# Optimization experiments

Hardware: AMD Instinct MI355X
Metric: run time of the kernel (lower is better)

Reference implementation:

```python
import jax, jax.numpy as jnp
import numpy as np

L = 3000          # nodes per modality
M = 3             # modalities
N = L * M         # total nodes
E = 200000        # edges
D = 512           # hidden_dim
S = D // 4        # shared_dim = 128
EPS = 1e-12       # F.normalize eps


def _lrelu(x):
    return jax.nn.leaky_relu(x, negative_slope=0.01)


def _l2norm(x):
    n = jnp.linalg.norm(x, axis=-1, keepdims=True)
    return x / jnp.maximum(n, EPS)


def setup_inputs() -> dict:
    key = jax.random.key(0)
    ks = jax.random.split(key, 16)
    w = lambda k, shape: (jax.random.normal(k, shape, dtype=jnp.float32) * 0.02)
    inp = {
        "feat0": jax.random.normal(ks[0], (L, D), dtype=jnp.float32),
        "feat1": jax.random.normal(ks[1], (L, D), dtype=jnp.float32),
        "feat2": jax.random.normal(ks[2], (L, D), dtype=jnp.float32),
        "edge_index": jax.random.randint(ks[3], (2, E), 0, N, dtype=jnp.int64),
        # EdgeWeightGen params (torch Linear convention: weight is (out, in))
        "proj_w": w(ks[4], (S, D)),
        "mlp_w1": w(ks[5], (S, 2 * S)),
        "mlp_b1": jnp.zeros((S,), dtype=jnp.float32),
        "mlp_w2": w(ks[6], (1, S)),
        "mlp_b2": jnp.zeros((1,), dtype=jnp.float32),
        # CrossModalGraphLayer params, 2 layers
        "W1_0": w(ks[7], (D, D)),
        "W2_0": w(ks[8], (D, 2 * D)),
        "W1_1": w(ks[9], (D, D)),
        "W2_1": w(ks[10], (D, 2 * D)),
    }
    return inp


def reference(feat0, feat1, feat2, edge_index, proj_w, mlp_w1, mlp_b1,
              mlp_w2, mlp_b2, W1_0, W2_0, W1_1, W2_1):
    feature = jnp.concatenate([feat0, feat1, feat2], axis=0)  # (N, D)
    src, tgt = edge_index[0], edge_index[1]

    # EdgeWeightGen
    shared_src = _l2norm(feature[src] @ proj_w.T)   # (E, S)
    shared_tgt = _l2norm(feature[tgt] @ proj_w.T)   # (E, S)
    emb_cat = jnp.concatenate([shared_src, shared_tgt], axis=-1)  # (E, 2S)
    h = _lrelu(emb_cat @ mlp_w1.T + mlp_b1)
    edge_weight = jax.nn.sigmoid((h @ mlp_w2.T + mlp_b2)[:, 0])   # (E,)

    # build_adj_matrix: dense scatter-add (sparse_coo coalesce sums dups)
    adj = jnp.zeros((N, N), dtype=feature.dtype).at[src, tgt].add(edge_weight)
    row_sum = adj.sum(axis=1)
    d_inv_sqrt = jnp.where(row_sum > 0, row_sum ** -0.5, 0.0)
    # D^{-1/2} A D^{-1/2} as elementwise row/col scaling (same math as diag matmuls)
    gcn = d_inv_sqrt[:, None] * adj * d_inv_sqrt[None, :]

    # graph layers
    x = feature
    for W1, W2 in ((W1_0, W2_0), (W1_1, W2_1)):
        proj = x @ W1.T                 # (N, D)
        nb = gcn @ proj                 # (N, D)
        cat = jnp.concatenate([x + nb, x * nb], axis=-1)  # (N, 2D)
        x = _lrelu(cat @ W2.T)
    return x  # concatenated updated features; chunk(x, 3) recovers per-modal tuple
```

## Files before the change

kernel.cpp:

```cpp
#include <hip/hip_runtime.h>
#include <hip/hip_bf16.h>
#include <math.h>

#define NL 3000
#define NN 9000
#define NE 200000
#define DD 512
#define SS 128
#define MPAD 9088
#define MT   (MPAD/16)

typedef __attribute__((ext_vector_type(8))) short    bf16x8;
typedef __attribute__((ext_vector_type(8))) ushort   u16x8;
typedef __attribute__((ext_vector_type(4))) float    f32x4;

static __device__ __forceinline__ ushort f2bf(float f){
  unsigned u = __float_as_uint(f);
  return (ushort)((u + 0x7FFFu + ((u>>16)&1u)) >> 16);
}
static __device__ __forceinline__ float bf2f(ushort u){
  return __uint_as_float(((unsigned)u)<<16);
}

__global__ __launch_bounds__(256) void k_cpack(const float* __restrict__ f0, const float* __restrict__ f1,
                                               const float* __restrict__ f2, short* __restrict__ P){
  int t = blockIdx.x*4 + (threadIdx.x>>6);
  int lane = threadIdx.x & 63;
  int tm = t >> 4, tk = t & 15;
  int m = tm*16 + (lane&15);
  int k = tk*32 + (lane>>4)*8;
  float4 v0 = make_float4(0,0,0,0), v1 = v0;
  if (m < NN){
    const float* srow = (m < NL) ? f0 + (size_t)m*DD
                       : (m < 2*NL) ? f1 + (size_t)(m-NL)*DD
                       : f2 + (size_t)(m-2*NL)*DD;
    v0 = *(const float4*)(srow + k);
    v1 = *(const float4*)(srow + k + 4);
  }
  u16x8 r;
  r[0]=f2bf(v0.x); r[1]=f2bf(v0.y); r[2]=f2bf(v0.z); r[3]=f2bf(v0.w);
  r[4]=f2bf(v1.x); r[5]=f2bf(v1.y); r[6]=f2bf(v1.z); r[7]=f2bf(v1.w);
  *(u16x8*)(P + (size_t)t*512 + lane*8) = r;
}

__global__ __launch_bounds__(256) void k_pack(const float* __restrict__ X, short* __restrict__ P,
                                              int M, int K, int nTilesK){
  int t = blockIdx.x*4 + (threadIdx.x>>6);
  int lane = threadIdx.x & 63;
  int tm = t / nTilesK, tk = t - tm*nTilesK;
  int m = tm*16 + (lane&15);
  int k = tk*32 + (lane>>4)*8;
  float4 v0 = make_float4(0,0,0,0), v1 = v0;
  if (m < M){
    v0 = *(const float4*)(X + (size_t)m*K + k);
    v1 = *(const float4*)(X + (size_t)m*K + k + 4);
  }
  u16x8 r;
  r[0]=f2bf(v0.x); r[1]=f2bf(v0.y); r[2]=f2bf(v0.z); r[3]=f2bf(v0.w);
  r[4]=f2bf(v1.x); r[5]=f2bf(v1.y); r[6]=f2bf(v1.z); r[7]=f2bf(v1.w);
  *(u16x8*)(P + (size_t)t*512 + lane*8) = r;
}

__global__ __launch_bounds__(256) void k_wpack5(const float* __restrict__ pw,
                                                const float* __restrict__ W10, const float* __restrict__ W20,
                                                const float* __restrict__ W11, const float* __restrict__ W21,
                                                short* __restrict__ BpF,
                                                short* __restrict__ Bp10, short* __restrict__ Bp20,
                                                short* __restrict__ Bp11, short* __restrict__ Bp21){
  int t = blockIdx.x*4 + (threadIdx.x>>6);
  int lane = threadIdx.x & 63;
  const float* X; short* P; int K, ntk, lt;
  if (t < 128)      { X=pw;  P=BpF;  K=512;  ntk=16; lt=t; }
  else if (t < 640) { X=W10; P=Bp10; K=512;  ntk=16; lt=t-128; }
  else if (t < 1664){ X=W20; P=Bp20; K=1024; ntk=32; lt=t-640; }
  else if (t < 2176){ X=W11; P=Bp11; K=512;  ntk=16; lt=t-1664; }
  else              { X=W21; P=Bp21; K=1024; ntk=32; lt=t-2176; }
  int tm = lt/ntk, tk = lt - tm*ntk;
  int m = tm*16 + (lane&15);
  int k = tk*32 + (lane>>4)*8;
  float4 v0 = *(const float4*)(X + (size_t)m*K + k);
  float4 v1 = *(const float4*)(X + (size_t)m*K + k + 4);
  u16x8 r;
  r[0]=f2bf(v0.x); r[1]=f2bf(v0.y); r[2]=f2bf(v0.z); r[3]=f2bf(v0.w);
  r[4]=f2bf(v1.x); r[5]=f2bf(v1.y); r[6]=f2bf(v1.z); r[7]=f2bf(v1.w);
  *(u16x8*)(P + (size_t)lt*512 + lane*8) = r;
}

__global__ __launch_bounds__(256) void k_pack_w1(const float* __restrict__ w1, short* __restrict__ P){
  int t = blockIdx.x*4 + (threadIdx.x>>6);
  int lane = threadIdx.x & 63;
  int tn = t >> 2, tk = t & 3;
  int n = tn*16 + (lane&15);
  int k = tk*32 + (lane>>4)*8;
  const float* sp = (n<128) ? (w1 + (size_t)n*256 + k) : (w1 + (size_t)(n-128)*256 + 128 + k);
  float4 v0 = *(const float4*)sp;
  float4 v1 = *(const float4*)(sp+4);
  u16x8 r;
  r[0]=f2bf(v0.x); r[1]=f2bf(v0.y); r[2]=f2bf(v0.z); r[3]=f2bf(v0.w);
  r[4]=f2bf(v1.x); r[5]=f2bf(v1.y); r[6]=f2bf(v1.z); r[7]=f2bf(v1.w);
  *(u16x8*)(P + (size_t)t*512 + lane*8) = r;
}

template<int ACT, int OBF>
__global__ __launch_bounds__(256) void k_gmm(const short* __restrict__ Ap, const short* __restrict__ Bp,
                                             void* __restrict__ Cv, int M, int N, int K){
  int lane = threadIdx.x & 63, wave = threadIdx.x >> 6;
  int ktiles = K >> 5;
  int bm = blockIdx.y*128 + wave*32;
  int bn = blockIdx.x*64;
  const bf16x8* a0 = (const bf16x8*)(Ap + ((size_t)((bm>>4)  ) * ktiles)*512 + lane*8);
  const bf16x8* a1 = (const bf16x8*)(Ap + ((size_t)((bm>>4)+1) * ktiles)*512 + lane*8);
  const bf16x8* b0 = (const bf16x8*)(Bp + ((size_t)((bn>>4)  ) * ktiles)*512 + lane*8);
  const bf16x8* b1 = (const bf16x8*)(Bp + ((size_t)((bn>>4)+1) * ktiles)*512 + lane*8);
  const bf16x8* b2 = (const bf16x8*)(Bp + ((size_t)((bn>>4)+2) * ktiles)*512 + lane*8);
  const bf16x8* b3 = (const bf16x8*)(Bp + ((size_t)((bn>>4)+3) * ktiles)*512 + lane*8);
  f32x4 acc[2][4];
  #pragma unroll
  for (int i=0;i<2;++i)
    #pragma unroll
    for (int j=0;j<4;++j) acc[i][j] = (f32x4){0.f,0.f,0.f,0.f};

  for (int kt=0; kt<ktiles; ++kt){
    int off = kt*64;
    bf16x8 A0 = a0[off], A1 = a1[off];
    bf16x8 B0 = b0[off], B1 = b1[off], B2 = b2[off], B3 = b3[off];
    acc[0][0] = __builtin_amdgcn_mfma_f32_16x16x32_bf16(A0, B0, acc[0][0], 0,0,0);
    acc[0][1] = __builtin_amdgcn_mfma_f32_16x16x32_bf16(A0, B1, acc[0][1], 0,0,0);
    acc[0][2] = __builtin_amdgcn_mfma_f32_16x16x32_bf16(A0, B2, acc[0][2], 0,0,0);
    acc[0][3] = __builtin_amdgcn_mfma_f32_16x16x32_bf16(A0, B3, acc[0][3], 0,0,0);
    acc[1][0] = __builtin_amdgcn_mfma_f32_16x16x32_bf16(A1, B0, acc[1][0], 0,0,0);
    acc[1][1] = __builtin_amdgcn_mfma_f32_16x16x32_bf16(A1, B1, acc[1][1], 0,0,0);
    acc[1][2] = __builtin_amdgcn_mfma_f32_16x16x32_bf16(A1, B2, acc[1][2], 0,0,0);
    acc[1][3] = __builtin_amdgcn_mfma_f32_16x16x32_bf16(A1, B3, acc[1][3], 0,0,0);
  }
  int colo = lane & 15;
  int rowo = (lane >> 4) * 4;
  #pragma unroll
  for (int mi=0; mi<2; ++mi){
    #pragma unroll
    for (int r=0; r<4; ++r){
      int row = bm + mi*16 + rowo + r;
      if (row < M){
        #pragma unroll
        for (int ni=0; ni<4; ++ni){
          float v = acc[mi][ni][r];
          if (ACT) v = v>0.f ? v : 0.01f*v;
          int cidx = bn + ni*16 + colo;
          if (OBF) ((ushort*)Cv)[(size_t)row*N + cidx] = f2bf(v);
          else     ((float*) Cv)[(size_t)row*N + cidx] = v;
        }
      }
    }
  }
}

__global__ __launch_bounds__(256) void k_l2n(const float* __restrict__ X, short* __restrict__ ShP){
  int lane = threadIdx.x & 63, wave = threadIdx.x >> 6;
  int m = blockIdx.x*4 + wave;
  float2 v = ((const float2*)(X + (size_t)m*SS))[lane];
  float ss = v.x*v.x + v.y*v.y;
  #pragma unroll
  for (int o=32;o>0;o>>=1) ss += __shfl_xor(ss, o);
  float inv = 1.f / fmaxf(sqrtf(ss), 1e-12f);
  int k = 2*lane;
  int tIdx = (m>>4)*4 + (k>>5);
  int pos  = ((m&15) + ((k>>3)&3)*16)*8 + (k&7);
  ushort2 r; r.x = f2bf(v.x*inv); r.y = f2bf(v.y*inv);
  *(ushort2*)(ShP + (size_t)tIdx*512 + pos) = r;
}

__global__ __launch_bounds__(256) void k_edge(const int* __restrict__ src, const int* __restrict__ tgt,
                      const ushort* __restrict__ AB,
                      const float* __restrict__ b1, const float* __restrict__ w2,
                      const float* __restrict__ b2p,
                      float* __restrict__ ew, float* __restrict__ row_sum, int* __restrict__ cnt){
  int lane = threadIdx.x & 63;
  int p = lane & 15, g = lane >> 4;
  int wid = blockIdx.x*(blockDim.x>>6) + (threadIdx.x>>6);
  int nw  = gridDim.x*(blockDim.x>>6);
  float4 b1a = ((const float4*)b1)[p*2], b1b = ((const float4*)b1)[p*2+1];
  float4 w2a = ((const float4*)w2)[p*2], w2b = ((const float4*)w2)[p*2+1];
  float bb[8] = {b1a.x,b1a.y,b1a.z,b1a.w,b1b.x,b1b.y,b1b.z,b1b.w};
  float ww[8] = {w2a.x,w2a.y,w2a.z,w2a.w,w2b.x,w2b.y,w2b.z,w2b.w};
  float b2 = b2p[0];
  for (int e = wid*4+g; e < NE; e += nw*4){
    int s = src[e], tg_ = tgt[e];
    u16x8 av = *(const u16x8*)(AB + (size_t)s*256 + p*8);
    u16x8 bv = *(const u16x8*)(AB + (size_t)tg_*256 + 128 + p*8);
    float acc = 0.f;
    #pragma unroll
    for (int i=0;i<8;++i){
      float h = bf2f(av[i]) + bf2f(bv[i]) + bb[i];
      h = h>0.f ? h : 0.01f*h;
      acc += h*ww[i];
    }
    acc += __shfl_xor(acc,1); acc += __shfl_xor(acc,2);
    acc += __shfl_xor(acc,4); acc += __shfl_xor(acc,8);
    if (p==0){
      float wgt = 1.f/(1.f+expf(-(acc+b2)));
      ew[e]=wgt;
      atomicAdd(&row_sum[s], wgt);
      atomicAdd(&cnt[s], 1);
    }
  }
}

__global__ __launch_bounds__(1024) void k_scan(const int* __restrict__ cnt, const float* __restrict__ row_sum,
                      int* __restrict__ row_ptr, float* __restrict__ dinv, int* __restrict__ fill){
  __shared__ int wsum[16];
  int t = threadIdx.x;
  int lane = t & 63, wid = t >> 6;
  const int CH = 9;
  int base = t*CH;
  int v[CH]; int s = 0;
  #pragma unroll
  for (int i=0;i<CH;++i){
    int idx = base+i;
    v[i] = (idx<NN) ? cnt[idx] : 0;
    s += v[i];
  }
  int ps = s;
  #pragma unroll
  for (int o=1;o<64;o<<=1){
    int x = __shfl_up(ps, o);
    if (lane >= o) ps += x;
  }
  if (lane==63) wsum[wid] = ps;
  __syncthreads();
  if (wid==0){
    int wv = (lane<16)? wsum[lane] : 0;
    #pragma unroll
    for (int o=1;o<16;o<<=1){
      int x = __shfl_up(wv, o);
      if (lane>=o) wv += x;
    }
    if (lane<16) wsum[lane]=wv;
  }
  __syncthreads();
  int prefix = (wid>0 ? wsum[wid-1] : 0) + (ps - s);
  #pragma unroll
  for (int i=0;i<CH;++i){
    int idx = base+i;
    if (idx<NN){
      row_ptr[idx] = prefix;
      float rs = row_sum[idx];
      dinv[idx] = rs>0.f ? (1.f/sqrtf(rs)) : 0.f;
      fill[idx] = 0;
      prefix += v[i];
    }
  }
  if (t==1023) row_ptr[NN] = wsum[15];
}

__global__ __launch_bounds__(256) void k_scatter(const int* __restrict__ src, const int* __restrict__ tgt,
                        const float* __restrict__ ew, const float* __restrict__ dinv,
                        const int* __restrict__ row_ptr, int* __restrict__ fill,
                        int* __restrict__ col, float* __restrict__ coef){
  int e = blockIdx.x*blockDim.x+threadIdx.x;
  if (e>=NE) return;
  int s=src[e], tg=tgt[e];
  int pos = atomicAdd(&fill[s],1);
  int idx = row_ptr[s]+pos;
  col[idx]=tg;
  coef[idx]=dinv[s]*ew[e]*dinv[tg];
}

template<int LAYER>
__global__ __launch_bounds__(128) void k_spmm_cat(const int* __restrict__ row_ptr, const int* __restrict__ col,
                     const float* __restrict__ coef, const ushort* __restrict__ proj,
                     const float* __restrict__ xf0, const float* __restrict__ xf1,
                     const float* __restrict__ xf2,
                     short* __restrict__ P){
  int m = blockIdx.x, t = threadIdx.x;
  int beg = row_ptr[m], end = row_ptr[m+1];
  float4 a0 = make_float4(0,0,0,0), a1 = a0, a2 = a0, a3 = a0;
  int j = beg;
  for (; j+4<=end; j+=4){
    int c0=col[j], c1=col[j+1], c2=col[j+2], c3=col[j+3];
    float w0=coef[j], w1=coef[j+1], w2_=coef[j+2], w3=coef[j+3];
    ushort4 p0 = ((const ushort4*)(proj + (size_t)c0*DD))[t];
    ushort4 p1 = ((const ushort4*)(proj + (size_t)c1*DD))[t];
    ushort4 p2 = ((const ushort4*)(proj + (size_t)c2*DD))[t];
    ushort4 p3 = ((const ushort4*)(proj + (size_t)c3*DD))[t];
    a0.x += w0*bf2f(p0.x); a0.y += w0*bf2f(p0.y); a0.z += w0*bf2f(p0.z); a0.w += w0*bf2f(p0.w);
    a1.x += w1*bf2f(p1.x); a1.y += w1*bf2f(p1.y); a1.z += w1*bf2f(p1.z); a1.w += w1*bf2f(p1.w);
    a2.x += w2_*bf2f(p2.x); a2.y += w2_*bf2f(p2.y); a2.z += w2_*bf2f(p2.z); a2.w += w2_*bf2f(p2.w);
    a3.x += w3*bf2f(p3.x); a3.y += w3*bf2f(p3.y); a3.z += w3*bf2f(p3.z); a3.w += w3*bf2f(p3.w);
  }
  for (; j<end; ++j){
    int c0=col[j]; float w0=coef[j];
    ushort4 p0 = ((const ushort4*)(proj + (size_t)c0*DD))[t];
    a0.x += w0*bf2f(p0.x); a0.y += w0*bf2f(p0.y); a0.z += w0*bf2f(p0.z); a0.w += w0*bf2f(p0.w);
  }
  a0.x += a1.x + a2.x + a3.x;
  a0.y += a1.y + a2.y + a3.y;
  a0.z += a1.z + a2.z + a3.z;
  a0.w += a1.w + a2.w + a3.w;
  const float* xrow;
  if (LAYER==0){
    xrow = (m < NL) ? xf0 + (size_t)m*DD
         : (m < 2*NL) ? xf1 + (size_t)(m-NL)*DD
         : xf2 + (size_t)(m-2*NL)*DD;
  } else {
    xrow = xf0 + (size_t)m*DD;
  }
  float4 xv = ((const float4*)xrow)[t];
  float ax = xv.x + a0.x, ay = xv.y + a0.y, az = xv.z + a0.z, aw = xv.w + a0.w;
  float mx = xv.x * a0.x, my = xv.y * a0.y, mz = xv.z * a0.z, mw = xv.w * a0.w;
  ushort4 ra, rm;
  ra.x=f2bf(ax); ra.y=f2bf(ay); ra.z=f2bf(az); ra.w=f2bf(aw);
  rm.x=f2bf(mx); rm.y=f2bf(my); rm.z=f2bf(mz); rm.w=f2bf(mw);
  size_t tileA = (size_t)((m>>4)*32 + (t>>3));
  int    off   = ((m&15) + ((t>>1)&3)*16)*8 + (t&1)*4;
  *(ushort4*)(P + tileA*512 + off)        = ra;
  *(ushort4*)(P + (tileA+16)*512 + off)   = rm;
}

extern "C" void kernel_launch(void* const* d_in, const int* in_sizes, int n_in,
                              void* d_out, int out_size, void* d_ws, size_t ws_size,
                              hipStream_t stream){
  const float* f0 = (const float*)d_in[0];
  const float* f1 = (const float*)d_in[1];
  const float* f2 = (const float*)d_in[2];
  const int*   ei = (const int*)d_in[3];
  const float* pw = (const float*)d_in[4];
  const float* w1 = (const float*)d_in[5];
  const float* b1 = (const float*)d_in[6];
  const float* w2 = (const float*)d_in[7];
  const float* b2 = (const float*)d_in[8];
  const float* W1_0 = (const float*)d_in[9];
  const float* W2_0 = (const float*)d_in[10];
  const float* W1_1 = (const float*)d_in[11];
  const float* W2_1 = (const float*)d_in[12];
  float* out = (float*)d_out;

  const int* src = ei;
  const int* tgt = ei + NE;

  char* base = (char*)d_ws;
  size_t o = 0;
  auto alloc = [&](size_t bytes)->char*{ char* p = base + o; o += (bytes + 1023) & ~size_t(1023); return p; };
  float* x1      = (float*)alloc((size_t)NN*DD*4);
  ushort* projbf = (ushort*)alloc((size_t)NN*DD*2);
  float* projS   = (float*)alloc((size_t)NN*SS*4);
  ushort* ABn    = (ushort*)alloc((size_t)NN*256*2);
  short* Apack1  = (short*)alloc((size_t)MT*16*1024);
  short* Apack2  = (short*)alloc((size_t)MT*32*1024);
  short* ShP     = (short*)alloc((size_t)MT*4*1024);
  short* BpF     = (short*)alloc((size_t)8*16*1024);
  short* Bpab    = (short*)alloc((size_t)16*4*1024);
  short* Bp10    = (short*)alloc((size_t)32*16*1024);
  short* Bp20    = (short*)alloc((size_t)32*32*1024);
  short* Bp11    = (short*)alloc((size_t)32*16*1024);
  short* Bp21    = (short*)alloc((size_t)32*32*1024);
  float* ew      = (float*)alloc(NE*4);
  float* coef    = (float*)alloc(NE*4);
  float* row_sum = (float*)alloc(NN*4);
  int*   cnt     = (int*)alloc(NN*4);
  float* dinv    = (float*)alloc(NN*4);
  int*   fill    = (int*)alloc(NN*4);
  int*   row_ptr = (int*)alloc((NN+1)*4);
  int*   col     = (int*)alloc(NE*4);

  hipMemsetAsync(row_sum, 0, NN*4, stream);
  hipMemsetAsync(cnt, 0, NN*4, stream);

  k_cpack<<<MT*16/4, 256, 0, stream>>>(f0,f1,f2,Apack1);
  k_wpack5<<<800, 256, 0, stream>>>(pw,W1_0,W2_0,W1_1,W2_1,BpF,Bp10,Bp20,Bp11,Bp21);
  k_pack_w1<<<16, 256, 0, stream>>>(w1, Bpab);

  dim3 gF(128/64, MPAD/128);
  k_gmm<0,0><<<gF, 256, 0, stream>>>(Apack1, BpF, projS, NN, 128, 512);
  k_l2n<<<NN/4, 256, 0, stream>>>(projS, ShP);
  dim3 gAB(256/64, MPAD/128);
  k_gmm<0,1><<<gAB, 256, 0, stream>>>(ShP, Bpab, ABn, NN, 256, 128);

  k_edge<<<2048, 256, 0, stream>>>(src,tgt,ABn,b1,w2,b2,ew,row_sum,cnt);
  k_scan<<<1, 1024, 0, stream>>>(cnt,row_sum,row_ptr,dinv,fill);
  k_scatter<<<(NE+255)/256, 256, 0, stream>>>(src,tgt,ew,dinv,row_ptr,fill,col,coef);

  dim3 gg(512/64, MPAD/128);
  k_gmm<0,1><<<gg, 256, 0, stream>>>(Apack1, Bp10, projbf, NN, DD, DD);
  k_spmm_cat<0><<<NN, 128, 0, stream>>>(row_ptr, col, coef, projbf, f0, f1, f2, Apack2);
  k_gmm<1,0><<<gg, 256, 0, stream>>>(Apack2, Bp20, x1, NN, DD, 2*DD);
  k_pack<<<MT*16/4, 256, 0, stream>>>(x1, Apack1, NN, DD, 16);
  k_gmm<0,1><<<gg, 256, 0, stream>>>(Apack1, Bp11, projbf, NN, DD, DD);
  k_spmm_cat<1><<<NN, 128, 0, stream>>>(row_ptr, col, coef, projbf, x1, nullptr, nullptr, Apack2);
  k_gmm<1,0><<<gg, 256, 0, stream>>>(Apack2, Bp21, out, NN, DD, 2*DD);
}
```

Measured before the change: 353.8 us.

## Merge pack kernels and memsets, fuse x1 repack into GEMM epilogue, share B via LDS

Folds the feature pack, the weight packs, the w1 pack and the row_sum/cnt memsets into one launch. The layer-0 output GEMM now also writes the bf16 MFMA-packed copy of x1, which removes the separate k_pack pass. The GEMM loads each B tile once per block into shared memory rather than once per wave. The trade-off is two __syncthreads per k-iteration with no double buffering, which may stall the MFMA pipeline, plus scattered 2-byte stores in the epilogue.

```diff
diff --git a/kernel.cpp b/kernel.cpp
--- a/kernel.cpp
+++ b/kernel.cpp
@@ -22,108 +22,97 @@
   return __uint_as_float(((unsigned)u)<<16);
 }
 
-__global__ __launch_bounds__(256) void k_cpack(const float* __restrict__ f0, const float* __restrict__ f1,
-                                               const float* __restrict__ f2, short* __restrict__ P){
-  int t = blockIdx.x*4 + (threadIdx.x>>6);
+__global__ __launch_bounds__(256) void k_packall(const float* __restrict__ f0, const float* __restrict__ f1,
+                        const float* __restrict__ f2, const float* __restrict__ pw,
+                        const float* __restrict__ w1,
+                        const float* __restrict__ W10, const float* __restrict__ W20,
+                        const float* __restrict__ W11, const float* __restrict__ W21,
+                        short* __restrict__ Ap1, short* __restrict__ BpF,
+                        short* __restrict__ Bp10, short* __restrict__ Bp20,
+                        short* __restrict__ Bp11, short* __restrict__ Bp21,
+                        short* __restrict__ Bpab,
+                        float* __restrict__ row_sum, int* __restrict__ cnt){
+  int b = blockIdx.x;
   int lane = threadIdx.x & 63;
-  int tm = t >> 4, tk = t & 15;
-  int m = tm*16 + (lane&15);
-  int k = tk*32 + (lane>>4)*8;
-  float4 v0 = make_float4(0,0,0,0), v1 = v0;
-  if (m < NN){
-    const float* srow = (m < NL) ? f0 + (size_t)m*DD
-                       : (m < 2*NL) ? f1 + (size_t)(m-NL)*DD
-                       : f2 + (size_t)(m-2*NL)*DD;
-    v0 = *(const float4*)(srow + k);
-    v1 = *(const float4*)(srow + k + 4);
-  }
-  u16x8 r;
-  r[0]=f2bf(v0.x); r[1]=f2bf(v0.y); r[2]=f2bf(v0.z); r[3]=f2bf(v0.w);
-  r[4]=f2bf(v1.x); r[5]=f2bf(v1.y); r[6]=f2bf(v1.z); r[7]=f2bf(v1.w);
-  *(u16x8*)(P + (size_t)t*512 + lane*8) = r;
-}
-
-__global__ __launch_bounds__(256) void k_pack(const float* __restrict__ X, short* __restrict__ P,
-                                              int M, int K, int nTilesK){
-  int t = blockIdx.x*4 + (threadIdx.x>>6);
-  int lane = threadIdx.x & 63;
-  int tm = t / nTilesK, tk = t - tm*nTilesK;
-  int m = tm*16 + (lane&15);
-  int k = tk*32 + (lane>>4)*8;
-  float4 v0 = make_float4(0,0,0,0), v1 = v0;
-  if (m < M){
-    v0 = *(const float4*)(X + (size_t)m*K + k);
-    v1 = *(const float4*)(X + (size_t)m*K + k + 4);
-  }
-  u16x8 r;
-  r[0]=f2bf(v0.x); r[1]=f2bf(v0.y); r[2]=f2bf(v0.z); r[3]=f2bf(v0.w);
-  r[4]=f2bf(v1.x); r[5]=f2bf(v1.y); r[6]=f2bf(v1.z); r[7]=f2bf(v1.w);
-  *(u16x8*)(P + (size_t)t*512 + lane*8) = r;
-}
-
-__global__ __launch_bounds__(256) void k_wpack5(const float* __restrict__ pw,
-                                                const float* __restrict__ W10, const float* __restrict__ W20,
-                                                const float* __restrict__ W11, const float* __restrict__ W21,
-                                                short* __restrict__ BpF,
-                                                short* __restrict__ Bp10, short* __restrict__ Bp20,
-                                                short* __restrict__ Bp11, short* __restrict__ Bp21){
-  int t = blockIdx.x*4 + (threadIdx.x>>6);
-  int lane = threadIdx.x & 63;
-  const float* X; short* P; int K, ntk, lt;
-  if (t < 128)      { X=pw;  P=BpF;  K=512;  ntk=16; lt=t; }
-  else if (t < 640) { X=W10; P=Bp10; K=512;  ntk=16; lt=t-128; }
-  else if (t < 1664){ X=W20; P=Bp20; K=1024; ntk=32; lt=t-640; }
-  else if (t < 2176){ X=W11; P=Bp11; K=512;  ntk=16; lt=t-1664; }
-  else              { X=W21; P=Bp21; K=1024; ntk=32; lt=t-2176; }
-  int tm = lt/ntk, tk = lt - tm*ntk;
-  int m = tm*16 + (lane&15);
-  int k = tk*32 + (lane>>4)*8;
-  float4 v0 = *(const float4*)(X + (size_t)m*K + k);
-  float4 v1 = *(const float4*)(X + (size_t)m*K + k + 4);
-  u16x8 r;
-  r[0]=f2bf(v0.x); r[1]=f2bf(v0.y); r[2]=f2bf(v0.z); r[3]=f2bf(v0.w);
-  r[4]=f2bf(v1.x); r[5]=f2bf(v1.y); r[6]=f2bf(v1.z); r[7]=f2bf(v1.w);
-  *(u16x8*)(P + (size_t)lt*512 + lane*8) = r;
-}
-
-__global__ __launch_bounds__(256) void k_pack_w1(const float* __restrict__ w1, short* __restrict__ P){
-  int t = blockIdx.x*4 + (threadIdx.x>>6);
-  int lane = threadIdx.x & 63;
-  int tn = t >> 2, tk = t & 3;
-  int n = tn*16 + (lane&15);
-  int k = tk*32 + (lane>>4)*8;
-  const float* sp = (n<128) ? (w1 + (size_t)n*256 + k) : (w1 + (size_t)(n-128)*256 + 128 + k);
-  float4 v0 = *(const float4*)sp;
-  float4 v1 = *(const float4*)(sp+4);
-  u16x8 r;
-  r[0]=f2bf(v0.x); r[1]=f2bf(v0.y); r[2]=f2bf(v0.z); r[3]=f2bf(v0.w);
-  r[4]=f2bf(v1.x); r[5]=f2bf(v1.y); r[6]=f2bf(v1.z); r[7]=f2bf(v1.w);
-  *(u16x8*)(P + (size_t)t*512 + lane*8) = r;
-}
-
-template<int ACT, int OBF>
+  if (b < 2272){
+    int t = b*4 + (threadIdx.x>>6);
+    int tm = t >> 4, tk = t & 15;
+    int m = tm*16 + (lane&15);
+    int k = tk*32 + (lane>>4)*8;
+    float4 v0 = make_float4(0,0,0,0), v1 = v0;
+    if (m < NN){
+      const float* srow = (m < NL) ? f0 + (size_t)m*DD
+                         : (m < 2*NL) ? f1 + (size_t)(m-NL)*DD
+                         : f2 + (size_t)(m-2*NL)*DD;
+      v0 = *(const float4*)(srow + k);
+      v1 = *(const float4*)(srow + k + 4);
+    }
+    u16x8 r;
+    r[0]=f2bf(v0.x); r[1]=f2bf(v0.y); r[2]=f2bf(v0.z); r[3]=f2bf(v0.w);
+    r[4]=f2bf(v1.x); r[5]=f2bf(v1.y); r[6]=f2bf(v1.z); r[7]=f2bf(v1.w);
+    *(u16x8*)(Ap1 + (size_t)t*512 + lane*8) = r;
+  } else if (b < 3072){
+    int t = (b-2272)*4 + (threadIdx.x>>6);
+    const float* X; short* P; int K, ntk, lt;
+    if (t < 128)      { X=pw;  P=BpF;  K=512;  ntk=16; lt=t; }
+    else if (t < 640) { X=W10; P=Bp10; K=512;  ntk=16; lt=t-128; }
+    else if (t < 1664){ X=W20; P=Bp20; K=1024; ntk=32; lt=t-640; }
+    else if (t < 2176){ X=W11; P=Bp11; K=512;  ntk=16; lt=t-1664; }
+    else              { X=W21; P=Bp21; K=1024; ntk=32; lt=t-2176; }
+    int tm = lt/ntk, tk = lt - tm*ntk;
+    int m = tm*16 + (lane&15);
+    int k = tk*32 + (lane>>4)*8;
+    float4 v0 = *(const float4*)(X + (size_t)m*K + k);
+    float4 v1 = *(const float4*)(X + (size_t)m*K + k + 4);
+    u16x8 r;
+    r[0]=f2bf(v0.x); r[1]=f2bf(v0.y); r[2]=f2bf(v0.z); r[3]=f2bf(v0.w);
+    r[4]=f2bf(v1.x); r[5]=f2bf(v1.y); r[6]=f2bf(v1.z); r[7]=f2bf(v1.w);
+    *(u16x8*)(P + (size_t)lt*512 + lane*8) = r;
+  } else if (b < 3088){
+    int t = (b-3072)*4 + (threadIdx.x>>6);
+    int tn = t >> 2, tk = t & 3;
+    int n = tn*16 + (lane&15);
+    int k = tk*32 + (lane>>4)*8;
+    const float* sp = (n<128) ? (w1 + (size_t)n*256 + k) : (w1 + (size_t)(n-128)*256 + 128 + k);
+    float4 v0 = *(const float4*)sp;
+    float4 v1 = *(const float4*)(sp+4);
+    u16x8 r;
+    r[0]=f2bf(v0.x); r[1]=f2bf(v0.y); r[2]=f2bf(v0.z); r[3]=f2bf(v0.w);
+    r[4]=f2bf(v1.x); r[5]=f2bf(v1.y); r[6]=f2bf(v1.z); r[7]=f2bf(v1.w);
+    *(u16x8*)(Bpab + (size_t)t*512 + lane*8) = r;
+  } else {
+    int idx = (b-3088)*256 + threadIdx.x;
+    for (int i=idx; i<NN; i+=4608){ row_sum[i]=0.f; cnt[i]=0; }
+  }
+}
+
+template<int ACT, int OBF, int OPK>
 __global__ __launch_bounds__(256) void k_gmm(const short* __restrict__ Ap, const short* __restrict__ Bp,
-                                             void* __restrict__ Cv, int M, int N, int K){
+                                             void* __restrict__ Cv, short* __restrict__ Pk,
+                                             int M, int N, int K){
+  __shared__ short Bs[2048];
   int lane = threadIdx.x & 63, wave = threadIdx.x >> 6;
   int ktiles = K >> 5;
   int bm = blockIdx.y*128 + wave*32;
   int bn = blockIdx.x*64;
   const bf16x8* a0 = (const bf16x8*)(Ap + ((size_t)((bm>>4)  ) * ktiles)*512 + lane*8);
   const bf16x8* a1 = (const bf16x8*)(Ap + ((size_t)((bm>>4)+1) * ktiles)*512 + lane*8);
-  const bf16x8* b0 = (const bf16x8*)(Bp + ((size_t)((bn>>4)  ) * ktiles)*512 + lane*8);
-  const bf16x8* b1 = (const bf16x8*)(Bp + ((size_t)((bn>>4)+1) * ktiles)*512 + lane*8);
-  const bf16x8* b2 = (const bf16x8*)(Bp + ((size_t)((bn>>4)+2) * ktiles)*512 + lane*8);
-  const bf16x8* b3 = (const bf16x8*)(Bp + ((size_t)((bn>>4)+3) * ktiles)*512 + lane*8);
+  const short*  bsrc = Bp + ((size_t)((bn>>4)+wave) * ktiles)*512 + lane*8;
   f32x4 acc[2][4];
   #pragma unroll
   for (int i=0;i<2;++i)
     #pragma unroll
     for (int j=0;j<4;++j) acc[i][j] = (f32x4){0.f,0.f,0.f,0.f};
 
+  const bf16x8* bsh = (const bf16x8*)Bs;
   for (int kt=0; kt<ktiles; ++kt){
+    u16x8 breg = *(const u16x8*)(bsrc + (size_t)kt*512);
+    __syncthreads();
+    *(u16x8*)&Bs[wave*512 + lane*8] = breg;
+    __syncthreads();
     int off = kt*64;
     bf16x8 A0 = a0[off], A1 = a1[off];
-    bf16x8 B0 = b0[off], B1 = b1[off], B2 = b2[off], B3 = b3[off];
+    bf16x8 B0 = bsh[lane], B1 = bsh[64+lane], B2 = bsh[128+lane], B3 = bsh[192+lane];
     acc[0][0] = __builtin_amdgcn_mfma_f32_16x16x32_bf16(A0, B0, acc[0][0], 0,0,0);
     acc[0][1] = __builtin_amdgcn_mfma_f32_16x16x32_bf16(A0, B1, acc[0][1], 0,0,0);
     acc[0][2] = __builtin_amdgcn_mfma_f32_16x16x32_bf16(A0, B2, acc[0][2], 0,0,0);
@@ -148,6 +137,11 @@
           int cidx = bn + ni*16 + colo;
           if (OBF) ((ushort*)Cv)[(size_t)row*N + cidx] = f2bf(v);
           else     ((float*) Cv)[(size_t)row*N + cidx] = v;
+          if (OPK){
+            size_t tl = (size_t)(row>>4)*16 + (cidx>>5);
+            int pos = ((row&15) + ((cidx>>3)&3)*16)*8 + (cidx&7);
+            Pk[tl*512 + pos] = (short)f2bf(v);
+          }
         }
       }
     }
@@ -362,29 +356,24 @@
   int*   row_ptr = (int*)alloc((NN+1)*4);
   int*   col     = (int*)alloc(NE*4);
 
-  hipMemsetAsync(row_sum, 0, NN*4, stream);
-  hipMemsetAsync(cnt, 0, NN*4, stream);
-
-  k_cpack<<<MT*16/4, 256, 0, stream>>>(f0,f1,f2,Apack1);
-  k_wpack5<<<800, 256, 0, stream>>>(pw,W1_0,W2_0,W1_1,W2_1,BpF,Bp10,Bp20,Bp11,Bp21);
-  k_pack_w1<<<16, 256, 0, stream>>>(w1, Bpab);
+  k_packall<<<3106, 256, 0, stream>>>(f0,f1,f2,pw,w1,W1_0,W2_0,W1_1,W2_1,
+                                      Apack1,BpF,Bp10,Bp20,Bp11,Bp21,Bpab,row_sum,cnt);
 
   dim3 gF(128/64, MPAD/128);
-  k_gmm<0,0><<<gF, 256, 0, stream>>>(Apack1, BpF, projS, NN, 128, 512);
+  k_gmm<0,0,0><<<gF, 256, 0, stream>>>(Apack1, BpF, projS, nullptr, NN, 128, 512);
   k_l2n<<<NN/4, 256, 0, stream>>>(projS, ShP);
   dim3 gAB(256/64, MPAD/128);
-  k_gmm<0,1><<<gAB, 256, 0, stream>>>(ShP, Bpab, ABn, NN, 256, 128);
+  k_gmm<0,1,0><<<gAB, 256, 0, stream>>>(ShP, Bpab, ABn, nullptr, NN, 256, 128);
 
   k_edge<<<2048, 256, 0, stream>>>(src,tgt,ABn,b1,w2,b2,ew,row_sum,cnt);
   k_scan<<<1, 1024, 0, stream>>>(cnt,row_sum,row_ptr,dinv,fill);
   k_scatter<<<(NE+255)/256, 256, 0, stream>>>(src,tgt,ew,dinv,row_ptr,fill,col,coef);
 
   dim3 gg(512/64, MPAD/128);
-  k_gmm<0,1><<<gg, 256, 0, stream>>>(Apack1, Bp10, projbf, NN, DD, DD);
+  k_gmm<0,1,0><<<gg, 256, 0, stream>>>(Apack1, Bp10, projbf, nullptr, NN, DD, DD);
   k_spmm_cat<0><<<NN, 128, 0, stream>>>(row_ptr, col, coef, projbf, f0, f1, f2, Apack2);
-  k_gmm<1,0><<<gg, 256, 0, stream>>>(Apack2, Bp20, x1, NN, DD, 2*DD);
-  k_pack<<<MT*16/4, 256, 0, stream>>>(x1, Apack1, NN, DD, 16);
-  k_gmm<0,1><<<gg, 256, 0, stream>>>(Apack1, Bp11, projbf, NN, DD, DD);
+  k_gmm<1,0,1><<<gg, 256, 0, stream>>>(Apack2, Bp20, x1, Apack1, NN, DD, 2*DD);
+  k_gmm<0,1,0><<<gg, 256, 0, stream>>>(Apack1, Bp11, projbf, nullptr, NN, DD, DD);
   k_spmm_cat<1><<<NN, 128, 0, stream>>>(row_ptr, col, coef, projbf, x1, nullptr, nullptr, Apack2);
-  k_gmm<1,0><<<gg, 256, 0, stream>>>(Apack2, Bp21, out, NN, DD, 2*DD);
-}
+  k_gmm<1,0,0><<<gg, 256, 0, stream>>>(Apack2, Bp21, out, nullptr, NN, DD, 2*DD);
+}
```

Result: no change. 360.2 us (+1.8%).
